# Kernel optimization log

Hardware: AMD Instinct MI355X
Metric: run time of the kernel (lower is better)

Reference implementation:

```python
import jax, jax.numpy as jnp
import numpy as np

B, R, D, H, L, E, NREL = 8, 1024, 256, 8, 2, 32768, 32
FF = 4 * D
HD = D // H
NEG = -1e9  # finite 'masked' value (stands in for -inf in the sparse attention mask)


def setup_inputs() -> dict:
    key = jax.random.key(0)
    ks = jax.random.split(key, 18)
    s = 0.02
    inp = {
        'node_embeddings': jax.random.normal(ks[0], (B, R, D), jnp.float32),
        'edge_index': jax.random.randint(ks[1], (B, 2, E), 0, R, jnp.int32),
        'relation_id': jax.random.randint(ks[2], (B, E), 0, NREL, jnp.int32),
        'keep_mask': jax.random.randint(ks[3], (B, E), 0, 2, jnp.int32).astype(bool),
        # learned params
        'rel_bias': jax.random.normal(ks[4], (max(NREL, 32), 1), jnp.float32) * s,
        'Wqkv': jax.random.normal(ks[5], (L, 3 * D, D), jnp.float32) * s,
        'bqkv': jnp.zeros((L, 3 * D), jnp.float32),
        'Wo': jax.random.normal(ks[6], (L, D, D), jnp.float32) * s,
        'bo': jnp.zeros((L, D), jnp.float32),
        'ln1_g': jnp.ones((L, D), jnp.float32),
        'ln1_b': jnp.zeros((L, D), jnp.float32),
        'W1': jax.random.normal(ks[7], (L, FF, D), jnp.float32) * s,
        'b1': jnp.zeros((L, FF), jnp.float32),
        'W2': jax.random.normal(ks[8], (L, D, FF), jnp.float32) * s,
        'b2': jnp.zeros((L, D), jnp.float32),
        'ln2_g': jnp.ones((L, D), jnp.float32),
        'ln2_b': jnp.zeros((L, D), jnp.float32),
    }
    return inp


def _layer_norm(x, g, b, eps=1e-5):
    mu = jnp.mean(x, axis=-1, keepdims=True)
    var = jnp.mean(jnp.square(x - mu), axis=-1, keepdims=True)
    return (x - mu) * jax.lax.rsqrt(var + eps) * g + b


def _build_mask(edge_index, relation_id, keep_mask, rel_bias):
    # Vectorized equivalent of the per-batch / per-edge Python loops:
    # base mask: NEG everywhere, 0 at kept edges (and diagonal), then scatter-ADD
    # the per-edge relation bias (duplicate edges accumulate, as in the loop).
    src = edge_index[:, 0, :]  # [B,E]
    dst = edge_index[:, 1, :]  # [B,E]
    bidx = jnp.broadcast_to(jnp.arange(B)[:, None], (B, E))
    mask = jnp.full((B, R, R), NEG, jnp.float32)
    base_vals = jnp.where(keep_mask, 0.0, NEG)
    mask = mask.at[bidx, src, dst].max(base_vals)  # dropped edges leave NEG
    di = jnp.arange(R)
    mask = mask.at[:, di, di].set(0.0)  # self-attention always allowed
    bias = rel_bias[relation_id, 0]  # [B,E]
    mask = mask.at[bidx, src, dst].add(jnp.where(keep_mask, bias, 0.0))
    return mask


def reference(node_embeddings, edge_index, relation_id, keep_mask, rel_bias,
              Wqkv, bqkv, Wo, bo, ln1_g, ln1_b, W1, b1, W2, b2, ln2_g, ln2_b):
    mask = _build_mask(edge_index, relation_id, keep_mask, rel_bias)  # [B,R,R]
    x = node_embeddings
    scale = 1.0 / np.sqrt(HD).astype(np.float32)
    for l in range(L):
        qkv = jnp.einsum('brd,ed->bre', x, Wqkv[l]) + bqkv[l]
        q, k, v = jnp.split(qkv, 3, axis=-1)
        q = q.reshape(B, R, H, HD)
        k = k.reshape(B, R, H, HD)
        v = v.reshape(B, R, H, HD)
        scores = jnp.einsum('bqhd,bkhd->bhqk', q, k) * scale + mask[:, None]
        attn = jax.nn.softmax(scores, axis=-1)
        out = jnp.einsum('bhqk,bkhd->bqhd', attn, v).reshape(B, R, D)
        out = jnp.einsum('brd,ed->bre', out, Wo[l]) + bo[l]
        x = _layer_norm(x + out, ln1_g[l], ln1_b[l])
        h = jax.nn.gelu(jnp.einsum('brd,fd->brf', x, W1[l]) + b1[l], approximate=False)
        h = jnp.einsum('brf,df->brd', h, W2[l]) + b2[l]
        x = _layer_norm(x + h, ln2_g[l], ln2_b[l])
    return x
```

## Files before the change

### kernel.cpp

```cpp
#include <hip/hip_runtime.h>
#include <hip/hip_bf16.h>
#include <math.h>

#define B_ 8
#define R_ 1024
#define D_ 256
#define H_ 8
#define L_ 2
#define E_ 32768
#define FF_ 1024
#define NEGV (-1000000000.0f)

typedef short bf16x8 __attribute__((ext_vector_type(8)));
typedef float f32x4 __attribute__((ext_vector_type(4)));

__device__ __forceinline__ unsigned short f2b(float f){
  unsigned int u = __float_as_uint(f);
  u += 0x7fffu + ((u >> 16) & 1u);
  return (unsigned short)(u >> 16);
}
__device__ __forceinline__ float b2f(unsigned short u){
  return __uint_as_float((unsigned int)u << 16);
}
__device__ __forceinline__ unsigned int pk_bf16(float lo, float hi){
  unsigned int r;
  asm volatile("v_cvt_pk_bf16_f32 %0, %1, %2" : "=v"(r) : "v"(lo), "v"(hi));
  return r;
}

#define ASYNC_COPY16(gp, lp) \
  __builtin_amdgcn_global_load_lds((const __attribute__((address_space(1))) void*)(gp), \
                                   (__attribute__((address_space(3))) void*)(lp), 16, 0, 0)


__global__ void detect_bool(const unsigned char* __restrict__ km, int* __restrict__ flag){
  int i = blockIdx.x*256 + threadIdx.x;
  int hit = ((i & 3) != 0) && (km[i] != 0);
  if (__ballot(hit) != 0ull && (threadIdx.x & 63) == 0) atomicOr(flag, 1);
}

__global__ void mask_fill(float* __restrict__ mask){
  size_t i = ((size_t)blockIdx.x*256 + threadIdx.x)*4;
  int row = (int)((i >> 10) & 1023);
  int col = (int)(i & 1023);
  float4 v;
  v.x = (row == col+0) ? 0.0f : NEGV;
  v.y = (row == col+1) ? 0.0f : NEGV;
  v.z = (row == col+2) ? 0.0f : NEGV;
  v.w = (row == col+3) ? 0.0f : NEGV;
  *(float4*)&mask[i] = v;
}

__device__ __forceinline__ int keep_of(const unsigned char* km, const int* flag, int tid){
  return flag[0] ? (int)km[tid] : (int)km[(size_t)tid*4];
}

__global__ void edge_base(const int* __restrict__ ei, const unsigned char* __restrict__ km,
                          const int* __restrict__ flag, float* __restrict__ mask){
  int tid = blockIdx.x*256 + threadIdx.x;
  int b = tid >> 15, e = tid & (E_-1);
  if (keep_of(km, flag, tid)){
    int src = ei[(size_t)b*2*E_ + e];
    int dst = ei[(size_t)b*2*E_ + E_ + e];
    mask[((size_t)b*R_ + src)*R_ + dst] = 0.0f;
  }
}

__global__ void edge_bias(const int* __restrict__ ei, const int* __restrict__ rid,
                          const unsigned char* __restrict__ km, const int* __restrict__ flag,
                          const float* __restrict__ rb, float* __restrict__ mask){
  int tid = blockIdx.x*256 + threadIdx.x;
  int b = tid >> 15, e = tid & (E_-1);
  if (keep_of(km, flag, tid)){
    int src = ei[(size_t)b*2*E_ + e];
    int dst = ei[(size_t)b*2*E_ + E_ + e];
    atomicAdd(&mask[((size_t)b*R_ + src)*R_ + dst], rb[rid[tid]]);
  }
}


__global__ void cvt_bf16(const float* __restrict__ src, unsigned short* __restrict__ dst, int n){
  int i = (blockIdx.x*256 + threadIdx.x)*4;
  if (i >= n) return;
  float4 v = *(const float4*)&src[i];
  ushort4 o;
  o.x = f2b(v.x); o.y = f2b(v.y); o.z = f2b(v.z); o.w = f2b(v.w);
  *(ushort4*)&dst[i] = o;
}

template<int MODE, int BN, int KS>
__global__ __launch_bounds__(256) void gemm_bt(const unsigned short* __restrict__ A,
    const unsigned short* __restrict__ Bw, const float* __restrict__ bias,
    void* __restrict__ Cout, int M, int N, int K)
{
  constexpr int NI = BN/32;
  constexpr int NCH = 8 + BN/16;
  constexpr int CPW = NCH/4;
  __shared__ unsigned short As[128*32];
  __shared__ unsigned short Bs[BN*32];
  const int nb = N / BN, mb = M >> 7;
  const int ks = blockIdx.x / (mb*nb);
  const int rem = blockIdx.x % (mb*nb);
  const int bm = rem / nb, bn = rem % nb;
  const int m0 = bm << 7, n0 = bn * BN;
  const int kbeg = ks * (K/KS), kend = kbeg + K/KS;
  const int t = threadIdx.x, lane = t & 63, wid = t >> 6;
  const int wr = wid >> 1, wc = wid & 1;
  const int c = lane & 15, g = lane >> 4;

  f32x4 zz = {0.f,0.f,0.f,0.f};
  f32x4 acc[4][NI];
  #pragma unroll
  for (int mi=0; mi<4; mi++)
    #pragma unroll
    for (int ni=0; ni<NI; ni++) acc[mi][ni] = zz;

  for (int k0 = kbeg; k0 < kend; k0 += 32){
    __syncthreads();
    #pragma unroll
    for (int it=0; it<CPW; ++it){
      int chunk = wid*CPW + it;
      int row16 = lane >> 2, seg = lane & 3;
      if (chunk < 8){
        int row = chunk*16 + row16;
        ASYNC_COPY16(A + (size_t)(m0+row)*K + k0 + seg*8, &As[chunk*512]);
      } else {
        int bch = chunk - 8;
        int row = bch*16 + row16;
        ASYNC_COPY16(Bw + (size_t)(n0+row)*K + k0 + seg*8, &Bs[bch*512]);
      }
    }
    __syncthreads();
    bf16x8 af[4], bfr[NI];
    #pragma unroll
    for (int mi=0; mi<4; mi++) af[mi]  = *(const bf16x8*)&As[(wr*64 + mi*16 + c)*32 + g*8];
    #pragma unroll
    for (int ni=0; ni<NI; ni++) bfr[ni] = *(const bf16x8*)&Bs[(wc*(BN/2) + ni*16 + c)*32 + g*8];
    #pragma unroll
    for (int mi=0; mi<4; mi++)
      #pragma unroll
      for (int ni=0; ni<NI; ni++)
        acc[mi][ni] = __builtin_amdgcn_mfma_f32_16x16x32_bf16(af[mi], bfr[ni], acc[mi][ni], 0,0,0);
  }

  unsigned short* outb = (unsigned short*)Cout + (size_t)ks*M*N;
  #pragma unroll
  for (int mi=0; mi<4; mi++){
    #pragma unroll
    for (int ni=0; ni<NI; ni++){
      int col = n0 + wc*(BN/2) + ni*16 + c;
      float bv = (MODE == 1) ? 0.0f : bias[col];
      #pragma unroll
      for (int r=0; r<4; r++){
        int row = m0 + wr*64 + mi*16 + 4*g + r;
        float v = acc[mi][ni][r] + bv;
        if (MODE == 2) v = 0.5f*v*(1.0f + erff(v*0.70710678f));
        outb[(size_t)row*N + col] = f2b(v);
      }
    }
  }
}

__global__ __launch_bounds__(512, 4) void attn_kernel(const unsigned short* __restrict__ qkv,
    const unsigned short* __restrict__ maskbf, unsigned short* __restrict__ po,
    float* __restrict__ ml)
{
  __shared__ unsigned short Klds[128*36];
  __shared__ unsigned short VT[32*132];
  const int blk = blockIdx.x;
  const int half = blk & 1, qt = (blk >> 1) & 7, h = (blk >> 4) & 7, b = blk >> 7;
  const int t = threadIdx.x, lane = t & 63, w = t >> 6;
  const int c = lane & 15, g = lane >> 4;
  const int qrow = qt*128 + w*16 + c;
  const size_t qbase = (size_t)b*R_*768;
  const float scale = 0.17677669529663689f;

  bf16x8 qf = *(const bf16x8*)&qkv[qbase + (size_t)qrow*768 + h*32 + g*8];

  f32x4 z4 = {0.f,0.f,0.f,0.f};
  f32x4 oacc[2] = {z4, z4};
  float mrun = -1e30f, lrun = 0.f;

  const int srcA = c + ((lane & 16) << 1);
  const int srcB = srcA + 16;
  const bool hig = (lane >= 32);

  for (int kt=0; kt<4; ++kt){
    const int kv0 = half*512 + kt*128;
    __syncthreads();
    {
      int row = t >> 2, seg = t & 3;
      uint4 kd = *(const uint4*)&qkv[qbase + (size_t)(kv0+row)*768 + 256 + h*32 + seg*8];
      *(uint4*)&Klds[row*36 + seg*8] = kd;
    }
    {
      int d = t & 31, grp = t >> 5;
      __align__(16) unsigned short tv[8];
      #pragma unroll
      for (int j=0; j<8; j++)
        tv[j] = qkv[qbase + (size_t)(kv0 + grp*8 + j)*768 + 512 + h*32 + d];
      *(uint4*)&VT[d*132 + grp*8] = *(const uint4*)&tv[0];
    }
    __syncthreads();

    f32x4 st[8];
    #pragma unroll
    for (int fc=0; fc<8; ++fc){
      bf16x8 kb = *(const bf16x8*)&Klds[(fc*16 + c)*36 + g*8];
      st[fc] = __builtin_amdgcn_mfma_f32_16x16x32_bf16(kb, qf, z4, 0,0,0);
    }
    const unsigned short* mrow = &maskbf[((size_t)b*R_ + qrow)*R_ + kv0];
    #pragma unroll
    for (int fc=0; fc<8; ++fc){
      ushort4 mu = *(const ushort4*)&mrow[fc*16 + 4*g];
      st[fc][0] = st[fc][0]*scale + b2f(mu.x);
      st[fc][1] = st[fc][1]*scale + b2f(mu.y);
      st[fc][2] = st[fc][2]*scale + b2f(mu.z);
      st[fc][3] = st[fc][3]*scale + b2f(mu.w);
    }
    float mx = st[0][0];
    #pragma unroll
    for (int fc=0; fc<8; ++fc)
      #pragma unroll
      for (int r=0; r<4; r++) mx = fmaxf(mx, st[fc][r]);
    mx = fmaxf(mx, __shfl_xor(mx, 16));
    mx = fmaxf(mx, __shfl_xor(mx, 32));
    float mnew  = fmaxf(mrun, mx);
    float alpha = __expf(mrun - mnew);
    float sum = 0.f;
    #pragma unroll
    for (int fc=0; fc<8; ++fc)
      #pragma unroll
      for (int r=0; r<4; r++){
        float pv = __expf(st[fc][r] - mnew);
        st[fc][r] = pv;
        sum += pv;
      }
    sum += __shfl_xor(sum, 16);
    sum += __shfl_xor(sum, 32);
    lrun = lrun*alpha + sum;
    mrun = mnew;
    oacc[0][0]*=alpha; oacc[0][1]*=alpha; oacc[0][2]*=alpha; oacc[0][3]*=alpha;
    oacc[1][0]*=alpha; oacc[1][1]*=alpha; oacc[1][2]*=alpha; oacc[1][3]*=alpha;

    unsigned int u0[8], u1[8];
    #pragma unroll
    for (int fc=0; fc<8; ++fc){
      u0[fc] = pk_bf16(st[fc][0], st[fc][1]);
      u1[fc] = pk_bf16(st[fc][2], st[fc][3]);
    }
    #pragma unroll
    for (int ks=0; ks<4; ++ks){
      unsigned int e0 = u0[2*ks],   e1 = u1[2*ks];
      unsigned int o0 = u0[2*ks+1], o1 = u1[2*ks+1];
      unsigned int w0e = __shfl((int)e0, srcA), w1e = __shfl((int)e1, srcA);
      unsigned int w2e = __shfl((int)e0, srcB), w3e = __shfl((int)e1, srcB);
      unsigned int w0o = __shfl((int)o0, srcA), w1o = __shfl((int)o1, srcA);
      unsigned int w2o = __shfl((int)o0, srcB), w3o = __shfl((int)o1, srcB);
      union { unsigned int u[4]; bf16x8 v; } pa;
      pa.u[0] = hig ? w0o : w0e;
      pa.u[1] = hig ? w1o : w1e;
      pa.u[2] = hig ? w2o : w2e;
      pa.u[3] = hig ? w3o : w3e;
      #pragma unroll
      for (int dg=0; dg<2; ++dg){
        bf16x8 vb = *(const bf16x8*)&VT[(dg*16 + c)*132 + ks*32 + g*8];
        oacc[dg] = __builtin_amdgcn_mfma_f32_16x16x32_bf16(vb, pa.v, oacc[dg], 0,0,0);
      }
    }
  }
  unsigned short* poh = po + (size_t)half*B_*R_*D_;
  #pragma unroll
  for (int dg=0; dg<2; ++dg){
    uint2 pp;
    pp.x = pk_bf16(oacc[dg][0], oacc[dg][1]);
    pp.y = pk_bf16(oacc[dg][2], oacc[dg][3]);
    *(uint2*)&poh[((size_t)b*R_ + qrow)*D_ + h*32 + dg*16 + 4*g] = pp;
  }
  if (g == 0){
    float2 v; v.x = mrun; v.y = lrun;
    *(float2*)&ml[((size_t)(half*64 + b*8 + h)*1024 + qrow)*2] = v;
  }
}

__global__ __launch_bounds__(256) void attn_merge(const unsigned short* __restrict__ po,
    const float* __restrict__ ml, unsigned short* __restrict__ aout)
{
  int idx = blockIdx.x*256 + threadIdx.x;
  int seg = idx & 3;
  int q   = (idx >> 2) & 1023;
  int h   = (idx >> 12) & 7;
  int b   = idx >> 15;
  size_t mlb = ((size_t)(b*8 + h)*1024 + q)*2;
  float m0 = ml[mlb],          l0 = ml[mlb + 1];
  float m1 = ml[131072 + mlb], l1 = ml[131072 + mlb + 1];
  float mm = fmaxf(m0, m1);
  float a0 = __expf(m0 - mm), a1 = __expf(m1 - mm);
  float inv = 1.0f / (a0*l0 + a1*l1);
  a0 *= inv; a1 *= inv;
  size_t base = ((size_t)b*R_ + q)*D_ + h*32 + seg*8;
  uint4 o0 = *(const uint4*)&po[base];
  uint4 o1 = *(const uint4*)&po[(size_t)B_*R_*D_ + base];
  uint4 out;
  unsigned int* p0 = (unsigned int*)&o0;
  unsigned int* p1 = (unsigned int*)&o1;
  unsigned int* po_ = (unsigned int*)&out;
  #pragma unroll
  for (int j=0; j<4; ++j){
    float lo = a0*__uint_as_float(p0[j] << 16)       + a1*__uint_as_float(p1[j] << 16);
    float hi = a0*__uint_as_float(p0[j] & 0xffff0000u) + a1*__uint_as_float(p1[j] & 0xffff0000u);
    po_[j] = pk_bf16(lo, hi);
  }
  *(uint4*)&aout[base] = out;
}

__global__ __launch_bounds__(256) void resid_ln3(const float* __restrict__ xin,
    const unsigned short* __restrict__ pA, const unsigned short* __restrict__ pB,
    const float* __restrict__ bias, const float* __restrict__ gg, const float* __restrict__ bb,
    float* __restrict__ xout, unsigned short* __restrict__ xbf)
{
  int row = blockIdx.x*4 + (threadIdx.x >> 6);
  int lane = threadIdx.x & 63;
  size_t base = (size_t)row*D_ + lane*4;
  float4 a  = *(const float4*)&xin[base];
  ushort4 ua = *(const ushort4*)&pA[base];
  ushort4 ub = *(const ushort4*)&pB[base];
  float4 bs = *(const float4*)&bias[lane*4];
  float y0 = a.x + b2f(ua.x) + b2f(ub.x) + bs.x;
  float y1 = a.y + b2f(ua.y) + b2f(ub.y) + bs.y;
  float y2 = a.z + b2f(ua.z) + b2f(ub.z) + bs.z;
  float y3 = a.w + b2f(ua.w) + b2f(ub.w) + bs.w;
  float s = y0+y1+y2+y3;
  #pragma unroll
  for (int off=32; off>=1; off>>=1) s += __shfl_xor(s, off);
  float mu = s * (1.0f/256.0f);
  float d0=y0-mu, d1=y1-mu, d2=y2-mu, d3=y3-mu;
  float q = d0*d0 + d1*d1 + d2*d2 + d3*d3;
  #pragma unroll
  for (int off=32; off>=1; off>>=1) q += __shfl_xor(q, off);
  float rstd = rsqrtf(q*(1.0f/256.0f) + 1e-5f);
  float4 gv = *(const float4*)&gg[lane*4];
  float4 bv = *(const float4*)&bb[lane*4];
  float o0 = d0*rstd*gv.x + bv.x;
  float o1 = d1*rstd*gv.y + bv.y;
  float o2 = d2*rstd*gv.z + bv.z;
  float o3 = d3*rstd*gv.w + bv.w;
  float4 o; o.x=o0; o.y=o1; o.z=o2; o.w=o3;
  *(float4*)&xout[base] = o;
  ushort4 ob; ob.x=f2b(o0); ob.y=f2b(o1); ob.z=f2b(o2); ob.w=f2b(o3);
  *(ushort4*)&xbf[base] = ob;
}

extern "C" void kernel_launch(void* const* d_in, const int* in_sizes, int n_in,
                              void* d_out, int out_size, void* d_ws, size_t ws_size,
                              hipStream_t stream)
{
  const float* node = (const float*)d_in[0];
  const int*   ei   = (const int*)d_in[1];
  const int*   rid  = (const int*)d_in[2];
  const unsigned char* km = (const unsigned char*)d_in[3];
  const float* rb   = (const float*)d_in[4];
  const float* Wqkv = (const float*)d_in[5];
  const float* bqkv = (const float*)d_in[6];
  const float* Wo   = (const float*)d_in[7];
  const float* bo   = (const float*)d_in[8];
  const float* ln1g = (const float*)d_in[9];
  const float* ln1b = (const float*)d_in[10];
  const float* W1   = (const float*)d_in[11];
  const float* b1   = (const float*)d_in[12];
  const float* W2   = (const float*)d_in[13];
  const float* b2   = (const float*)d_in[14];
  const float* ln2g = (const float*)d_in[15];
  const float* ln2b = (const float*)d_in[16];

  char* ws = (char*)d_ws;
  int*   flag   = (int*)ws;
  float* maskf  = (float*)(ws + 256);
  unsigned short* hbuf   = (unsigned short*)(ws + 256);
  unsigned short* maskbf = (unsigned short*)(ws + 33554688);
  unsigned short* wqkv_b = (unsigned short*)(ws + 50331904);
  unsigned short* wo_b   = (unsigned short*)(ws + 51118336);
  unsigned short* w1_b   = (unsigned short*)(ws + 51380480);
  unsigned short* w2_b   = (unsigned short*)(ws + 52429056);
  unsigned short* x_bf   = (unsigned short*)(ws + 53477632);
  unsigned short* qkvb   = (unsigned short*)(ws + 57671936);
  unsigned short* ao     = (unsigned short*)(ws + 57671936);
  float* xf   = (float*)(ws + 70254848);
  unsigned short* po  = (unsigned short*)(ws + 78643456);
  unsigned short* tmp = (unsigned short*)(ws + 78643456);
  float* ml   = (float*)(ws + 87032064);

  hipMemsetAsync(flag, 0, 4, stream);
  detect_bool<<<1024, 256, 0, stream>>>(km, flag);
  mask_fill<<<8192, 256, 0, stream>>>(maskf);
  edge_base<<<1024, 256, 0, stream>>>(ei, km, flag, maskf);
  edge_bias<<<1024, 256, 0, stream>>>(ei, rid, km, flag, rb, maskf);
  cvt_bf16<<<8192, 256, 0, stream>>>(maskf, maskbf, B_*R_*R_);

  cvt_bf16<<<384, 256, 0, stream>>>(Wqkv, wqkv_b, L_*768*256);
  cvt_bf16<<<128, 256, 0, stream>>>(Wo,   wo_b,   L_*256*256);
  cvt_bf16<<<512, 256, 0, stream>>>(W1,   w1_b,   L_*1024*256);
  cvt_bf16<<<512, 256, 0, stream>>>(W2,   w2_b,   L_*256*1024);
  cvt_bf16<<<2048,256, 0, stream>>>(node, x_bf,   B_*R_*D_);

  for (int l = 0; l < L_; ++l){
    gemm_bt<0,128,1><<<384, 256, 0, stream>>>(x_bf, wqkv_b + l*196608, bqkv + l*768, qkvb, 8192, 768, 256);
    attn_kernel<<<1024, 512, 0, stream>>>(qkvb, maskbf, po, ml);
    attn_merge<<<1024, 256, 0, stream>>>(po, ml, ao);
    gemm_bt<1,64,2><<<512, 256, 0, stream>>>(ao, wo_b + l*65536, bo + l*256, tmp, 8192, 256, 256);
    resid_ln3<<<2048, 256, 0, stream>>>(l==0 ? node : xf, tmp, tmp + 8192*256,
                                        bo + l*256, ln1g + l*256, ln1b + l*256, xf, x_bf);
    gemm_bt<2,128,1><<<512, 256, 0, stream>>>(x_bf, w1_b + l*262144, b1 + l*1024, hbuf, 8192, 1024, 256);
    gemm_bt<1,64,2><<<512, 256, 0, stream>>>(hbuf, w2_b + l*262144, b2 + l*256, tmp, 8192, 256, 1024);
    float* outp = (l == L_-1) ? (float*)d_out : xf;
    resid_ln3<<<2048, 256, 0, stream>>>(xf, tmp, tmp + 8192*256,
                                        b2 + l*256, ln2g + l*256, ln2b + l*256, outp, x_bf);
  }
}
```

Baseline: 359.2 us.

## Drop split-KV attention merge, double-buffer K/V tiles, fuse bf16 conversions

The attention kernel now walks all 1024 keys in one block instead of splitting keys across two blocks, so the separate merge kernel and the partial-output and max/sum buffers are gone. K/V tiles are double-buffered in LDS, with the next tile's global loads and mask values issued before the current tile is computed. The six bf16 conversion launches are merged into one kernel. In exchange there are half as many attention blocks, which reduces parallelism, and register pressure rises from the prefetched K, V and mask data.

```diff
diff --git a/kernel.cpp b/kernel.cpp
--- a/kernel.cpp
+++ b/kernel.cpp
@@ -78,14 +78,26 @@
   }
 }
 
-
-__global__ void cvt_bf16(const float* __restrict__ src, unsigned short* __restrict__ dst, int n){
-  int i = (blockIdx.x*256 + threadIdx.x)*4;
-  if (i >= n) return;
-  float4 v = *(const float4*)&src[i];
+__global__ __launch_bounds__(256) void cvt_all(const float* __restrict__ maskf,
+    const float* __restrict__ node, const float* __restrict__ Wqkv,
+    const float* __restrict__ Wo, const float* __restrict__ W1, const float* __restrict__ W2,
+    unsigned short* __restrict__ maskbf, unsigned short* __restrict__ x_bf,
+    unsigned short* __restrict__ wqkv_b, unsigned short* __restrict__ wo_b,
+    unsigned short* __restrict__ w1_b, unsigned short* __restrict__ w2_b)
+{
+  int bid = blockIdx.x;
+  const float* s; unsigned short* d; int base;
+  if      (bid < 8192)  { s = maskf; d = maskbf; base = bid; }
+  else if (bid < 10240) { s = node;  d = x_bf;   base = bid - 8192; }
+  else if (bid < 10624) { s = Wqkv;  d = wqkv_b; base = bid - 10240; }
+  else if (bid < 10752) { s = Wo;    d = wo_b;   base = bid - 10624; }
+  else if (bid < 11264) { s = W1;    d = w1_b;   base = bid - 10752; }
+  else                  { s = W2;    d = w2_b;   base = bid - 11264; }
+  size_t i = ((size_t)base*256 + threadIdx.x)*4;
+  float4 v = *(const float4*)&s[i];
   ushort4 o;
   o.x = f2b(v.x); o.y = f2b(v.y); o.z = f2b(v.z); o.w = f2b(v.w);
-  *(ushort4*)&dst[i] = o;
+  *(ushort4*)&d[i] = o;
 }
 
 template<int MODE, int BN, int KS>
@@ -161,62 +173,80 @@
   }
 }
 
-__global__ __launch_bounds__(512, 4) void attn_kernel(const unsigned short* __restrict__ qkv,
-    const unsigned short* __restrict__ maskbf, unsigned short* __restrict__ po,
-    float* __restrict__ ml)
+__global__ __launch_bounds__(512, 2) void attn_kernel(const unsigned short* __restrict__ qkv,
+    const unsigned short* __restrict__ maskbf, unsigned short* __restrict__ aout)
 {
-  __shared__ unsigned short Klds[128*36];
-  __shared__ unsigned short VT[32*132];
+  __shared__ unsigned short K0[128*36], K1[128*36];
+  __shared__ unsigned short V0[32*132], V1[32*132];
   const int blk = blockIdx.x;
-  const int half = blk & 1, qt = (blk >> 1) & 7, h = (blk >> 4) & 7, b = blk >> 7;
+  const int qt = blk & 7, h = (blk >> 3) & 7, b = blk >> 6;
   const int t = threadIdx.x, lane = t & 63, w = t >> 6;
   const int c = lane & 15, g = lane >> 4;
   const int qrow = qt*128 + w*16 + c;
   const size_t qbase = (size_t)b*R_*768;
   const float scale = 0.17677669529663689f;
 
+  const int krow = t >> 2, kseg = t & 3;
+  const int vd = t & 31, vgrp = t >> 5;
+
   bf16x8 qf = *(const bf16x8*)&qkv[qbase + (size_t)qrow*768 + h*32 + g*8];
 
   f32x4 z4 = {0.f,0.f,0.f,0.f};
   f32x4 oacc[2] = {z4, z4};
   float mrun = -1e30f, lrun = 0.f;
-
   const int srcA = c + ((lane & 16) << 1);
   const int srcB = srcA + 16;
   const bool hig = (lane >= 32);
 
-  for (int kt=0; kt<4; ++kt){
-    const int kv0 = half*512 + kt*128;
-    __syncthreads();
-    {
-      int row = t >> 2, seg = t & 3;
-      uint4 kd = *(const uint4*)&qkv[qbase + (size_t)(kv0+row)*768 + 256 + h*32 + seg*8];
-      *(uint4*)&Klds[row*36 + seg*8] = kd;
-    }
-    {
-      int d = t & 31, grp = t >> 5;
-      __align__(16) unsigned short tv[8];
-      #pragma unroll
-      for (int j=0; j<8; j++)
-        tv[j] = qkv[qbase + (size_t)(kv0 + grp*8 + j)*768 + 512 + h*32 + d];
-      *(uint4*)&VT[d*132 + grp*8] = *(const uint4*)&tv[0];
-    }
-    __syncthreads();
+  const unsigned short* mrowp = &maskbf[((size_t)b*R_ + qrow)*R_];
+
+  unsigned short* klW = K0; unsigned short* vtW = V0;
+  unsigned short* klR = K1; unsigned short* vtR = V1;
+
+  {
+    uint4 kd = *(const uint4*)&qkv[qbase + (size_t)krow*768 + 256 + h*32 + kseg*8];
+    __align__(16) unsigned short tv[8];
+    #pragma unroll
+    for (int j=0; j<8; j++) tv[j] = qkv[qbase + (size_t)(vgrp*8 + j)*768 + 512 + h*32 + vd];
+    *(uint4*)&klW[krow*36 + kseg*8] = kd;
+    *(uint4*)&vtW[vd*132 + vgrp*8] = *(const uint4*)&tv[0];
+  }
+  ushort4 mreg[8];
+  #pragma unroll
+  for (int fc=0; fc<8; ++fc) mreg[fc] = *(const ushort4*)&mrowp[fc*16 + 4*g];
+  __syncthreads();
+
+  for (int kt=0; kt<8; ++kt){
+    { unsigned short* x_ = klR; klR = klW; klW = x_; }
+    { unsigned short* x_ = vtR; vtR = vtW; vtW = x_; }
+    const bool more = (kt < 7);
+
+    uint4 kd;
+    __align__(16) unsigned short tv[8];
+    if (more){
+      const int kv1 = (kt+1)*128;
+      kd = *(const uint4*)&qkv[qbase + (size_t)(kv1+krow)*768 + 256 + h*32 + kseg*8];
+      #pragma unroll
+      for (int j=0; j<8; j++) tv[j] = qkv[qbase + (size_t)(kv1 + vgrp*8 + j)*768 + 512 + h*32 + vd];
+    }
 
     f32x4 st[8];
     #pragma unroll
     for (int fc=0; fc<8; ++fc){
-      bf16x8 kb = *(const bf16x8*)&Klds[(fc*16 + c)*36 + g*8];
+      bf16x8 kb = *(const bf16x8*)&klR[(fc*16 + c)*36 + g*8];
       st[fc] = __builtin_amdgcn_mfma_f32_16x16x32_bf16(kb, qf, z4, 0,0,0);
     }
-    const unsigned short* mrow = &maskbf[((size_t)b*R_ + qrow)*R_ + kv0];
     #pragma unroll
     for (int fc=0; fc<8; ++fc){
-      ushort4 mu = *(const ushort4*)&mrow[fc*16 + 4*g];
+      ushort4 mu = mreg[fc];
       st[fc][0] = st[fc][0]*scale + b2f(mu.x);
       st[fc][1] = st[fc][1]*scale + b2f(mu.y);
       st[fc][2] = st[fc][2]*scale + b2f(mu.z);
       st[fc][3] = st[fc][3]*scale + b2f(mu.w);
+    }
+    if (more){
+      #pragma unroll
+      for (int fc=0; fc<8; ++fc) mreg[fc] = *(const ushort4*)&mrowp[(kt+1)*128 + fc*16 + 4*g];
     }
     float mx = st[0][0];
     #pragma unroll
@@ -264,54 +294,27 @@
       pa.u[3] = hig ? w3o : w3e;
       #pragma unroll
       for (int dg=0; dg<2; ++dg){
-        bf16x8 vb = *(const bf16x8*)&VT[(dg*16 + c)*132 + ks*32 + g*8];
+        bf16x8 vb = *(const bf16x8*)&vtR[(dg*16 + c)*132 + ks*32 + g*8];
         oacc[dg] = __builtin_amdgcn_mfma_f32_16x16x32_bf16(vb, pa.v, oacc[dg], 0,0,0);
       }
     }
-  }
-  unsigned short* poh = po + (size_t)half*B_*R_*D_;
+
+    __syncthreads();
+    if (more){
+      *(uint4*)&klW[krow*36 + kseg*8] = kd;
+      *(uint4*)&vtW[vd*132 + vgrp*8] = *(const uint4*)&tv[0];
+    }
+    __syncthreads();
+  }
+
+  float rl = 1.0f / lrun;
   #pragma unroll
   for (int dg=0; dg<2; ++dg){
     uint2 pp;
-    pp.x = pk_bf16(oacc[dg][0], oacc[dg][1]);
-    pp.y = pk_bf16(oacc[dg][2], oacc[dg][3]);
-    *(uint2*)&poh[((size_t)b*R_ + qrow)*D_ + h*32 + dg*16 + 4*g] = pp;
-  }
-  if (g == 0){
-    float2 v; v.x = mrun; v.y = lrun;
-    *(float2*)&ml[((size_t)(half*64 + b*8 + h)*1024 + qrow)*2] = v;
-  }
-}
-
-__global__ __launch_bounds__(256) void attn_merge(const unsigned short* __restrict__ po,
-    const float* __restrict__ ml, unsigned short* __restrict__ aout)
-{
-  int idx = blockIdx.x*256 + threadIdx.x;
-  int seg = idx & 3;
-  int q   = (idx >> 2) & 1023;
-  int h   = (idx >> 12) & 7;
-  int b   = idx >> 15;
-  size_t mlb = ((size_t)(b*8 + h)*1024 + q)*2;
-  float m0 = ml[mlb],          l0 = ml[mlb + 1];
-  float m1 = ml[131072 + mlb], l1 = ml[131072 + mlb + 1];
-  float mm = fmaxf(m0, m1);
-  float a0 = __expf(m0 - mm), a1 = __expf(m1 - mm);
-  float inv = 1.0f / (a0*l0 + a1*l1);
-  a0 *= inv; a1 *= inv;
-  size_t base = ((size_t)b*R_ + q)*D_ + h*32 + seg*8;
-  uint4 o0 = *(const uint4*)&po[base];
-  uint4 o1 = *(const uint4*)&po[(size_t)B_*R_*D_ + base];
-  uint4 out;
-  unsigned int* p0 = (unsigned int*)&o0;
-  unsigned int* p1 = (unsigned int*)&o1;
-  unsigned int* po_ = (unsigned int*)&out;
-  #pragma unroll
-  for (int j=0; j<4; ++j){
-    float lo = a0*__uint_as_float(p0[j] << 16)       + a1*__uint_as_float(p1[j] << 16);
-    float hi = a0*__uint_as_float(p0[j] & 0xffff0000u) + a1*__uint_as_float(p1[j] & 0xffff0000u);
-    po_[j] = pk_bf16(lo, hi);
-  }
-  *(uint4*)&aout[base] = out;
+    pp.x = pk_bf16(oacc[dg][0]*rl, oacc[dg][1]*rl);
+    pp.y = pk_bf16(oacc[dg][2]*rl, oacc[dg][3]*rl);
+    *(uint2*)&aout[((size_t)b*R_ + qrow)*D_ + h*32 + dg*16 + 4*g] = pp;
+  }
 }
 
 __global__ __launch_bounds__(256) void resid_ln3(const float* __restrict__ xin,
@@ -377,6 +380,7 @@
   int*   flag   = (int*)ws;
   float* maskf  = (float*)(ws + 256);
   unsigned short* hbuf   = (unsigned short*)(ws + 256);
+  unsigned short* ao     = (unsigned short*)(ws + 16777472);
   unsigned short* maskbf = (unsigned short*)(ws + 33554688);
   unsigned short* wqkv_b = (unsigned short*)(ws + 50331904);
   unsigned short* wo_b   = (unsigned short*)(ws + 51118336);
@@ -384,29 +388,20 @@
   unsigned short* w2_b   = (unsigned short*)(ws + 52429056);
   unsigned short* x_bf   = (unsigned short*)(ws + 53477632);
   unsigned short* qkvb   = (unsigned short*)(ws + 57671936);
-  unsigned short* ao     = (unsigned short*)(ws + 57671936);
   float* xf   = (float*)(ws + 70254848);
-  unsigned short* po  = (unsigned short*)(ws + 78643456);
   unsigned short* tmp = (unsigned short*)(ws + 78643456);
-  float* ml   = (float*)(ws + 87032064);
 
   hipMemsetAsync(flag, 0, 4, stream);
   detect_bool<<<1024, 256, 0, stream>>>(km, flag);
   mask_fill<<<8192, 256, 0, stream>>>(maskf);
   edge_base<<<1024, 256, 0, stream>>>(ei, km, flag, maskf);
   edge_bias<<<1024, 256, 0, stream>>>(ei, rid, km, flag, rb, maskf);
-  cvt_bf16<<<8192, 256, 0, stream>>>(maskf, maskbf, B_*R_*R_);
-
-  cvt_bf16<<<384, 256, 0, stream>>>(Wqkv, wqkv_b, L_*768*256);
-  cvt_bf16<<<128, 256, 0, stream>>>(Wo,   wo_b,   L_*256*256);
-  cvt_bf16<<<512, 256, 0, stream>>>(W1,   w1_b,   L_*1024*256);
-  cvt_bf16<<<512, 256, 0, stream>>>(W2,   w2_b,   L_*256*1024);
-  cvt_bf16<<<2048,256, 0, stream>>>(node, x_bf,   B_*R_*D_);
+  cvt_all<<<11776, 256, 0, stream>>>(maskf, node, Wqkv, Wo, W1, W2,
+                                     maskbf, x_bf, wqkv_b, wo_b, w1_b, w2_b);
 
   for (int l = 0; l < L_; ++l){
     gemm_bt<0,128,1><<<384, 256, 0, stream>>>(x_bf, wqkv_b + l*196608, bqkv + l*768, qkvb, 8192, 768, 256);
-    attn_kernel<<<1024, 512, 0, stream>>>(qkvb, maskbf, po, ml);
-    attn_merge<<<1024, 256, 0, stream>>>(po, ml, ao);
+    attn_kernel<<<512, 512, 0, stream>>>(qkvb, maskbf, ao);
     gemm_bt<1,64,2><<<512, 256, 0, stream>>>(ao, wo_b + l*65536, bo + l*256, tmp, 8192, 256, 256);
     resid_ln3<<<2048, 256, 0, stream>>>(l==0 ? node : xf, tmp, tmp + 8192*256,
                                         bo + l*256, ln1g + l*256, ln1b + l*256, xf, x_bf);
```

After: 418.4 us. 16.5% more time.
